# Optimization experiments

Hardware: AMD Instinct MI355X
Metric: run time of the kernel (lower is better)

The kernel has to match this reference:

```python
import jax, jax.numpy as jnp
import numpy as np

N_NODES = 100000
N_EDGES = 1600000
IN, HID, OUT = 32, 32, 16


def setup_inputs() -> dict:
    key = jax.random.key(0)
    ks = jax.random.split(key, 8)
    return {
        "features": jax.random.normal(ks[0], (N_NODES, IN), dtype=jnp.float32),
        "src": jax.random.randint(ks[1], (N_EDGES,), 0, N_NODES, dtype=jnp.int32),
        "dst": jax.random.randint(ks[2], (N_EDGES,), 0, N_NODES, dtype=jnp.int32),
        "edge_weight": jax.random.uniform(ks[3], (N_EDGES,), dtype=jnp.float32),
        "W1": jax.random.normal(ks[4], (IN, HID), dtype=jnp.float32) * 0.1,
        "b1": jnp.zeros((HID,), dtype=jnp.float32),
        "W2": jax.random.normal(ks[5], (HID, OUT), dtype=jnp.float32) * 0.1,
        "b2": jnp.zeros((OUT,), dtype=jnp.float32),
    }


def _graph_conv(h, W, b, src, dst, edge_weight, norm_src, norm_dst, n):
    # DGL GraphConv, norm='both', with edge_weight (u_mul_e aggregation)
    h = h * norm_src[:, None]          # out-degree^-0.5 on source side
    h = h @ W                          # dense transform (tiny GEMM)
    m = h[src] * edge_weight[:, None]  # gather + edge weighting  [E, d]
    agg = jax.ops.segment_sum(m, dst, num_segments=n)  # scatter-add SpMM
    return agg * norm_dst[:, None] + b # in-degree^-0.5 + bias


def reference(features, src, dst, edge_weight, W1, b1, W2, b2):
    n = features.shape[0]
    ones_e = jnp.ones_like(edge_weight)
    deg_out = jnp.clip(jax.ops.segment_sum(ones_e, src, num_segments=n), 1.0)
    deg_in = jnp.clip(jax.ops.segment_sum(ones_e, dst, num_segments=n), 1.0)
    norm_src = deg_out ** -0.5
    norm_dst = deg_in ** -0.5
    h = _graph_conv(features, W1, b1, src, dst, edge_weight, norm_src, norm_dst, n)
    h = jax.nn.relu(h)
    # dropout is identity in eval mode
    h = _graph_conv(h, W2, b2, src, dst, edge_weight, norm_src, norm_dst, n)
    return h
```

## Files before the change

### kernel.cpp

```cpp
#include <hip/hip_runtime.h>
#include <hip/hip_fp16.h>


#define NB   391
#define CAPB 5504
#define EPB  4096

__device__ __forceinline__ long nt_load_i64(const long* p) {
    return __builtin_nontemporal_load(p);
}

__global__ __launch_bounds__(1024) void partition_kernel(
        const int* __restrict__ src, const int* __restrict__ dst,
        const float* __restrict__ ew,
        int* __restrict__ g_cur_d, int* __restrict__ g_cur_s,
        int2* __restrict__ pack_part, unsigned char* __restrict__ src_part, int m) {
    __shared__ int hist_d[NB], hist_s[NB];
    __shared__ int lbase_d[NB], lbase_s[NB];
    __shared__ int gbase_d[NB], gbase_s[NB];
    __shared__ int cur_d[NB], cur_s[NB];
    __shared__ int woffd[16], woffs[16];
    __shared__ long stage[EPB];
    __shared__ unsigned short dbuck[EPB];
    __shared__ unsigned char  sstage[EPB];
    __shared__ unsigned short sbuck[EPB];
    int t = threadIdx.x, lane = t & 63, w = t >> 6;
    for (int i = t; i < NB; i += 1024) {
        hist_d[i] = 0; hist_s[i] = 0; cur_d[i] = 0; cur_s[i] = 0;
    }
    __syncthreads();
    int base_e = blockIdx.x * EPB;
    int total = m - base_e; if (total > EPB) total = EPB;
    int es[4], ed[4]; float wv[4];
#pragma unroll
    for (int k = 0; k < 4; k++) {
        int e = base_e + k * 1024 + t;
        if (e < m) { es[k] = src[e]; ed[k] = dst[e]; wv[k] = ew[e]; }
        else ed[k] = -1;
    }
#pragma unroll
    for (int k = 0; k < 4; k++) {
        if (ed[k] >= 0) {
            atomicAdd(&hist_d[ed[k] >> 8], 1);
            atomicAdd(&hist_s[es[k] >> 8], 1);
        }
    }
    __syncthreads();
    int hvd = (t < NB) ? hist_d[t] : 0;
    int hvs = (t < NB) ? hist_s[t] : 0;
    int vd = hvd, vs = hvs;
#pragma unroll
    for (int off = 1; off < 64; off <<= 1) {
        int ud = __shfl_up(vd, off, 64);
        int us = __shfl_up(vs, off, 64);
        if (lane >= off) { vd += ud; vs += us; }
    }
    if (lane == 63) { woffd[w] = vd; woffs[w] = vs; }
    __syncthreads();
    if (t < 64) {
        int sd = (t < 16) ? woffd[t] : 0;
        int ss = (t < 16) ? woffs[t] : 0;
        int od = sd, os = ss;
#pragma unroll
        for (int off = 1; off < 16; off <<= 1) {
            int ud = __shfl_up(sd, off, 64);
            int us = __shfl_up(ss, off, 64);
            if (lane >= off) { sd += ud; ss += us; }
        }
        if (t < 16) { woffd[t] = sd - od; woffs[t] = ss - os; }
    }
    __syncthreads();
    if (t < NB) {
        lbase_d[t] = vd + woffd[w] - hvd;
        lbase_s[t] = vs + woffs[w] - hvs;
    }
    for (int i = t; i < NB; i += 1024) {
        int c = hist_d[i];
        gbase_d[i] = i * CAPB + (c ? atomicAdd(&g_cur_d[i], c) : 0);
        c = hist_s[i];
        gbase_s[i] = i * CAPB + (c ? atomicAdd(&g_cur_s[i], c) : 0);
    }
    __syncthreads();
#pragma unroll
    for (int k = 0; k < 4; k++) {
        if (ed[k] >= 0) {
            int d = ed[k], s = es[k];
            int bd = d >> 8;
            int r = atomicAdd(&cur_d[bd], 1);
            int pos = lbase_d[bd] + r;
            stage[pos] = (long)(unsigned int)(s | ((d & 255) << 20)) |
                         ((long)__float_as_int(wv[k]) << 32);
            dbuck[pos] = (unsigned short)bd;
            int bs = s >> 8;
            int rs = atomicAdd(&cur_s[bs], 1);
            int ps = lbase_s[bs] + rs;
            sstage[ps] = (unsigned char)(s & 255);
            sbuck[ps] = (unsigned short)bs;
        }
    }
    __syncthreads();
    long* packl = (long*)pack_part;
    for (int i = t; i < total; i += 1024) {
        int b = dbuck[i];
        packl[(size_t)gbase_d[b] + (i - lbase_d[b])] = stage[i];
    }
    for (int i = t; i < total; i += 1024) {
        int b = sbuck[i];
        src_part[(size_t)gbase_s[b] + (i - lbase_s[b])] = sstage[i];
    }
}

__global__ __launch_bounds__(1024) void csr_kernel(
                           const int2* __restrict__ pack_part,
                           const unsigned char* __restrict__ src_part,
                           const int* __restrict__ g_cur_d, const int* __restrict__ g_cur_s,
                           const float* __restrict__ feat, const float* __restrict__ W1,
                           int2* __restrict__ csr, int2* __restrict__ rs_cnt,
                           float* __restrict__ norm_src, float* __restrict__ norm_dst,
                           __half* __restrict__ h1, int n) {
    __shared__ int cnt[256];
    __shared__ int rowx[256];
    __shared__ int cur[256];
    __shared__ int cnt_s[256];
    __shared__ float nsrc[256];
    __shared__ float sW1[1024];
    extern __shared__ int2 stage[];
    int t = threadIdx.x, b = blockIdx.x;
    if (t < 256) { cnt[t] = 0; cur[t] = 0; cnt_s[t] = 0; }
    sW1[t] = W1[t];
    __syncthreads();
    int count = g_cur_d[b]; if (count > CAPB) count = CAPB;
    int count_s = g_cur_s[b]; if (count_s > CAPB) count_s = CAPB;
    const int2* p = pack_part + (size_t)b * CAPB;
    const unsigned char* sp = src_part + (size_t)b * CAPB;
    int2 pk[4];
#pragma unroll
    for (int u = 0; u < 4; u++) {
        int e = t + u * 1024;
        if (e < count) { pk[u] = p[e]; atomicAdd(&cnt[pk[u].x >> 20], 1); }
    }
    for (int e = t + 4096; e < count; e += 1024)
        atomicAdd(&cnt[p[e].x >> 20], 1);
    for (int e = t; e < count_s; e += 1024) atomicAdd(&cnt_s[sp[e]], 1);
    __syncthreads();
    if (t < 256) {
        int node = b * 256 + t;
        if (node < n) {
            int cs = cnt_s[t];
            float ns = rsqrtf((float)(cs > 1 ? cs : 1));
            nsrc[t] = ns;
            norm_src[node] = ns;
        } else nsrc[t] = 0.0f;
    }
    if (t < 64) {
        int c0 = cnt[t * 4], c1 = cnt[t * 4 + 1], c2 = cnt[t * 4 + 2], c3 = cnt[t * 4 + 3];
        int tot = c0 + c1 + c2 + c3;
        int incl = tot;
#pragma unroll
        for (int off = 1; off < 64; off <<= 1) {
            int u = __shfl_up(incl, off, 64);
            if (t >= off) incl += u;
        }
        int excl = incl - tot;
        rowx[t * 4]     = excl;
        rowx[t * 4 + 1] = excl + c0;
        rowx[t * 4 + 2] = excl + c0 + c1;
        rowx[t * 4 + 3] = excl + c0 + c1 + c2;
    }
    __syncthreads();
    if (t < 256) {
        int node = b * 256 + t;
        if (node < n) {
            rs_cnt[node] = make_int2(b * CAPB + rowx[t], cnt[t]);
            norm_dst[node] = rsqrtf((float)(cnt[t] > 1 ? cnt[t] : 1));
        }
    }
    __syncthreads();
#pragma unroll
    for (int u = 0; u < 4; u++) {
        int e = t + u * 1024;
        if (e < count) {
            int2 v = pk[u];
            int dl = v.x >> 20;
            int r = atomicAdd(&cur[dl], 1);
            stage[rowx[dl] + r] = make_int2(v.x & 0x1FFFF, v.y);
        }
    }
    for (int e = t + 4096; e < count; e += 1024) {
        int2 v = p[e];
        int dl = v.x >> 20;
        int r = atomicAdd(&cur[dl], 1);
        stage[rowx[dl] + r] = make_int2(v.x & 0x1FFFF, v.y);
    }
    __syncthreads();
    int2* outp = csr + (size_t)b * CAPB;
    for (int e = t; e < count; e += 1024) outp[e] = stage[e];
    __syncthreads();
    float* sF = (float*)stage;
    int node0 = b * 256;
    int lim = n - node0; if (lim > 256) lim = 256; if (lim < 0) lim = 0;
    for (int o = t; o < lim * 32; o += 1024) {
        int i = o >> 5, k = o & 31;
        sF[o] = feat[(size_t)(node0 + i) * 32 + k] * nsrc[i];
    }
    __syncthreads();
    for (int o = t; o < lim * 32; o += 1024) {
        int i = o >> 5, col = o & 31;
        float acc = 0.0f;
#pragma unroll
        for (int k = 0; k < 32; k++) acc += sF[i * 32 + k] * sW1[k * 32 + col];
        h1[(size_t)(node0 + i) * 32 + col] = __float2half(acc);
    }
}

__global__ void gather1_fused_kernel(const __half* __restrict__ h1, const int2* __restrict__ csr,
                                     const int2* __restrict__ rs_cnt,
                                     const float* __restrict__ norm_src, const float* __restrict__ norm_dst,
                                     const float* __restrict__ W2, const float* __restrict__ b1,
                                     __half* __restrict__ h2, int n) {
    __shared__ float sW2[32 * 16];
    __shared__ float sB1[32];
    __shared__ float sX[4][8][33];
    int t = threadIdx.x;
    for (int i = t; i < 512; i += 256) sW2[i] = W2[i];
    if (t < 32) sB1[t] = b1[t];
    __syncthreads();
    int w = t >> 6, lane = t & 63;
    int q = lane >> 3;
    int dq = lane & 7;
    int node = (blockIdx.x * 4 + w) * 8 + q;
    bool valid = node < n;
    int2 rc = valid ? rs_cnt[node] : make_int2(0, 0);
    long base = rc.x;
    int c = rc.y;
    const float2* tv = (const float2*)h1;
    const long* csrl = (const long*)csr;
    float a00=0,a01=0,a02=0,a03=0, a10=0,a11=0,a12=0,a13=0;
    float a20=0,a21=0,a22=0,a23=0, a30=0,a31=0,a32=0,a33=0;
    int j = 0;
    for (; j + 3 < c; j += 4) {
        long q0 = nt_load_i64(csrl + base + j);
        long q1 = nt_load_i64(csrl + base + j + 1);
        long q2 = nt_load_i64(csrl + base + j + 2);
        long q3 = nt_load_i64(csrl + base + j + 3);
        float2 r0 = tv[(size_t)((int)q0 & 0xFFFFF) * 8 + dq];
        float2 r1 = tv[(size_t)((int)q1 & 0xFFFFF) * 8 + dq];
        float2 r2 = tv[(size_t)((int)q2 & 0xFFFFF) * 8 + dq];
        float2 r3 = tv[(size_t)((int)q3 & 0xFFFFF) * 8 + dq];
        float w0 = __int_as_float((int)(q0 >> 32)), w1 = __int_as_float((int)(q1 >> 32));
        float w2 = __int_as_float((int)(q2 >> 32)), w3 = __int_as_float((int)(q3 >> 32));
        float2 l0 = __half22float2(*(__half2*)&r0.x), h0 = __half22float2(*(__half2*)&r0.y);
        float2 l1 = __half22float2(*(__half2*)&r1.x), h1v = __half22float2(*(__half2*)&r1.y);
        float2 l2 = __half22float2(*(__half2*)&r2.x), h2v = __half22float2(*(__half2*)&r2.y);
        float2 l3 = __half22float2(*(__half2*)&r3.x), h3v = __half22float2(*(__half2*)&r3.y);
        a00 += l0.x * w0; a01 += l0.y * w0; a02 += h0.x * w0; a03 += h0.y * w0;
        a10 += l1.x * w1; a11 += l1.y * w1; a12 += h1v.x * w1; a13 += h1v.y * w1;
        a20 += l2.x * w2; a21 += l2.y * w2; a22 += h2v.x * w2; a23 += h2v.y * w2;
        a30 += l3.x * w3; a31 += l3.y * w3; a32 += h3v.x * w3; a33 += h3v.y * w3;
    }
    for (; j < c; j++) {
        long qq = nt_load_i64(csrl + base + j);
        float2 r = tv[(size_t)((int)qq & 0xFFFFF) * 8 + dq];
        float ww = __int_as_float((int)(qq >> 32));
        float2 l = __half22float2(*(__half2*)&r.x), h = __half22float2(*(__half2*)&r.y);
        a00 += l.x * ww; a01 += l.y * ww; a02 += h.x * ww; a03 += h.y * ww;
    }
    float s0 = (a00 + a10) + (a20 + a30);
    float s1 = (a01 + a11) + (a21 + a31);
    float s2 = (a02 + a12) + (a22 + a32);
    float s3 = (a03 + a13) + (a23 + a33);
    if (valid) {
        float nd = norm_dst[node], ns = norm_src[node];
        int d0 = 4 * dq;
        sX[w][q][d0]     = fmaxf(s0 * nd + sB1[d0],     0.0f) * ns;
        sX[w][q][d0 + 1] = fmaxf(s1 * nd + sB1[d0 + 1], 0.0f) * ns;
        sX[w][q][d0 + 2] = fmaxf(s2 * nd + sB1[d0 + 2], 0.0f) * ns;
        sX[w][q][d0 + 3] = fmaxf(s3 * nd + sB1[d0 + 3], 0.0f) * ns;
    }
    if (valid) {
        float o0 = 0.0f, o1 = 0.0f;
        int c0 = 2 * dq, c1 = 2 * dq + 1;
#pragma unroll
        for (int k = 0; k < 32; k++) {
            float x = sX[w][q][k];
            o0 += x * sW2[k * 16 + c0];
            o1 += x * sW2[k * 16 + c1];
        }
        ((__half2*)h2)[(size_t)node * 8 + dq] = __floats2half2_rn(o0, o1);
    }
}

__global__ void gather2_kernel(const __half* __restrict__ h2, const int2* __restrict__ csr,
                               const int2* __restrict__ rs_cnt,
                               const float* __restrict__ norm_dst, const float* __restrict__ b2,
                               float* __restrict__ out, int n) {
    int t = threadIdx.x;
    int w = t >> 6, lane = t & 63;
    int q = lane >> 2;
    int dq = lane & 3;
    int node = (blockIdx.x * 4 + w) * 16 + q;
    bool valid = node < n;
    int2 rc = valid ? rs_cnt[node] : make_int2(0, 0);
    long base = rc.x;
    int c = rc.y;
    const float2* tv = (const float2*)h2;
    const long* csrl = (const long*)csr;
    float a00=0,a01=0,a02=0,a03=0, a10=0,a11=0,a12=0,a13=0;
    float a20=0,a21=0,a22=0,a23=0, a30=0,a31=0,a32=0,a33=0;
    int j = 0;
    for (; j + 3 < c; j += 4) {
        long q0 = nt_load_i64(csrl + base + j);
        long q1 = nt_load_i64(csrl + base + j + 1);
        long q2 = nt_load_i64(csrl + base + j + 2);
        long q3 = nt_load_i64(csrl + base + j + 3);
        float2 r0 = tv[(size_t)((int)q0 & 0xFFFFF) * 4 + dq];
        float2 r1 = tv[(size_t)((int)q1 & 0xFFFFF) * 4 + dq];
        float2 r2 = tv[(size_t)((int)q2 & 0xFFFFF) * 4 + dq];
        float2 r3 = tv[(size_t)((int)q3 & 0xFFFFF) * 4 + dq];
        float w0 = __int_as_float((int)(q0 >> 32)), w1 = __int_as_float((int)(q1 >> 32));
        float w2 = __int_as_float((int)(q2 >> 32)), w3 = __int_as_float((int)(q3 >> 32));
        float2 l0 = __half22float2(*(__half2*)&r0.x), h0 = __half22float2(*(__half2*)&r0.y);
        float2 l1 = __half22float2(*(__half2*)&r1.x), h1v = __half22float2(*(__half2*)&r1.y);
        float2 l2 = __half22float2(*(__half2*)&r2.x), h2v = __half22float2(*(__half2*)&r2.y);
        float2 l3 = __half22float2(*(__half2*)&r3.x), h3v = __half22float2(*(__half2*)&r3.y);
        a00 += l0.x * w0; a01 += l0.y * w0; a02 += h0.x * w0; a03 += h0.y * w0;
        a10 += l1.x * w1; a11 += l1.y * w1; a12 += h1v.x * w1; a13 += h1v.y * w1;
        a20 += l2.x * w2; a21 += l2.y * w2; a22 += h2v.x * w2; a23 += h2v.y * w2;
        a30 += l3.x * w3; a31 += l3.y * w3; a32 += h3v.x * w3; a33 += h3v.y * w3;
    }
    for (; j < c; j++) {
        long qq = nt_load_i64(csrl + base + j);
        float2 r = tv[(size_t)((int)qq & 0xFFFFF) * 4 + dq];
        float ww = __int_as_float((int)(qq >> 32));
        float2 l = __half22float2(*(__half2*)&r.x), h = __half22float2(*(__half2*)&r.y);
        a00 += l.x * ww; a01 += l.y * ww; a02 += h.x * ww; a03 += h.y * ww;
    }
    if (valid) {
        float nd = norm_dst[node];
        int d0 = 4 * dq;
        float4 o;
        o.x = ((a00 + a10) + (a20 + a30)) * nd + b2[d0];
        o.y = ((a01 + a11) + (a21 + a31)) * nd + b2[d0 + 1];
        o.z = ((a02 + a12) + (a22 + a32)) * nd + b2[d0 + 2];
        o.w = ((a03 + a13) + (a23 + a33)) * nd + b2[d0 + 3];
        ((float4*)out)[(size_t)node * 4 + dq] = o;
    }
}

extern "C" void kernel_launch(void* const* d_in, const int* in_sizes, int n_in,
                              void* d_out, int out_size, void* d_ws, size_t ws_size,
                              hipStream_t stream) {
    const float* feat = (const float*)d_in[0];
    const int*   src  = (const int*)d_in[1];
    const int*   dst  = (const int*)d_in[2];
    const float* ew   = (const float*)d_in[3];
    const float* W1   = (const float*)d_in[4];
    const float* b1   = (const float*)d_in[5];
    const float* W2   = (const float*)d_in[6];
    const float* b2   = (const float*)d_in[7];
    float* out = (float*)d_out;

    const int n = in_sizes[0] / 32;
    const int m = in_sizes[1];

    char* wsb = (char*)d_ws;
    int2*   pack_part = (int2*)wsb;
    int2*   csr       = pack_part + (size_t)NB * CAPB;
    __half* h1        = (__half*)(csr + (size_t)NB * CAPB);
    __half* h2        = h1 + 32 * (size_t)n;
    float*  norm_src  = (float*)(h2 + 16 * (size_t)n);
    float*  norm_dst  = norm_src + n;
    int2*   rs_cnt    = (int2*)(norm_dst + n);
    int*    g_cur_d   = (int*)(rs_cnt + n);
    int*    g_cur_s   = g_cur_d + NB;
    unsigned char* src_part = (unsigned char*)(g_cur_s + NB);

    hipMemsetAsync(g_cur_d, 0, 2 * NB * sizeof(int), stream);

    partition_kernel<<<(m + EPB - 1) / EPB, 1024, 0, stream>>>(src, dst, ew, g_cur_d, g_cur_s,
                                                               pack_part, src_part, m);
    csr_kernel<<<NB, 1024, CAPB * sizeof(int2), stream>>>(pack_part, src_part, g_cur_d, g_cur_s,
                                                          feat, W1, csr, rs_cnt,
                                                          norm_src, norm_dst, h1, n);
    gather1_fused_kernel<<<(n + 31) / 32, 256, 0, stream>>>(h1, csr, rs_cnt,
                                                            norm_src, norm_dst, W2, b1, h2, n);
    gather2_kernel<<<(n + 63) / 64, 256, 0, stream>>>(h2, csr, rs_cnt, norm_dst, b2, out, n);
}
```

Before: 186.8 us.

## Fuse GCN pipeline into one cooperative persistent kernel with LDS-resident CSR

Replaces the four separate kernels (partition, CSR build, two gather layers) with a single cooperative kernel of 256 persistent blocks separated by grid-wide syncs. Each block owns two destination buckets and keeps their CSR chains, degree counts and norms in LDS, so the global CSR, rs_cnt and norm arrays are no longer written or read. Layer 2 also runs the W2 transform inside the block. This removes launch gaps and global round-trips, at the cost of large dynamic LDS (about 88 KB) per block, fewer blocks in flight for the latency-bound gathers, and grid-sync overhead.

```diff
diff --git a/kernel.cpp b/kernel.cpp
--- a/kernel.cpp
+++ b/kernel.cpp
@@ -1,388 +1,401 @@
 #include <hip/hip_runtime.h>
 #include <hip/hip_fp16.h>
+#include <hip/hip_cooperative_groups.h>
+
+namespace cg = cooperative_groups;
 
 
 #define NB   391
 #define CAPB 5504
 #define EPB  4096
-
-__device__ __forceinline__ long nt_load_i64(const long* p) {
-    return __builtin_nontemporal_load(p);
-}
-
-__global__ __launch_bounds__(1024) void partition_kernel(
+#define NBLK 256
+#define TPB  1024
+#define UNIB (2 * CAPB * 8)
+
+__global__ __launch_bounds__(TPB, 4) void gcn_mega(
         const int* __restrict__ src, const int* __restrict__ dst,
-        const float* __restrict__ ew,
+        const float* __restrict__ ew, const float* __restrict__ feat,
+        const float* __restrict__ W1, const float* __restrict__ b1,
+        const float* __restrict__ W2, const float* __restrict__ b2,
         int* __restrict__ g_cur_d, int* __restrict__ g_cur_s,
-        int2* __restrict__ pack_part, unsigned char* __restrict__ src_part, int m) {
+        int2* __restrict__ pack_part, unsigned char* __restrict__ src_part,
+        __half* __restrict__ h1, __half* __restrict__ h2,
+        float* __restrict__ out, int n, int m) {
+    extern __shared__ __align__(16) char uni[];
     __shared__ int hist_d[NB], hist_s[NB];
     __shared__ int lbase_d[NB], lbase_s[NB];
     __shared__ int gbase_d[NB], gbase_s[NB];
     __shared__ int cur_d[NB], cur_s[NB];
     __shared__ int woffd[16], woffs[16];
-    __shared__ long stage[EPB];
-    __shared__ unsigned short dbuck[EPB];
-    __shared__ unsigned char  sstage[EPB];
-    __shared__ unsigned short sbuck[EPB];
-    int t = threadIdx.x, lane = t & 63, w = t >> 6;
-    for (int i = t; i < NB; i += 1024) {
-        hist_d[i] = 0; hist_s[i] = 0; cur_d[i] = 0; cur_s[i] = 0;
-    }
-    __syncthreads();
-    int base_e = blockIdx.x * EPB;
-    int total = m - base_e; if (total > EPB) total = EPB;
-    int es[4], ed[4]; float wv[4];
-#pragma unroll
-    for (int k = 0; k < 4; k++) {
-        int e = base_e + k * 1024 + t;
-        if (e < m) { es[k] = src[e]; ed[k] = dst[e]; wv[k] = ew[e]; }
-        else ed[k] = -1;
-    }
-#pragma unroll
-    for (int k = 0; k < 4; k++) {
-        if (ed[k] >= 0) {
-            atomicAdd(&hist_d[ed[k] >> 8], 1);
-            atomicAdd(&hist_s[es[k] >> 8], 1);
+    __shared__ int cnt[2][256], rowx[2][256], cura[256], cnt_s[256];
+    __shared__ float nsrc[2][256], ndst[2][256];
+    __shared__ float sW1[1024], sW2[512], sB1[32], sB2[16];
+    __shared__ float sX[16][8][33];
+
+    cg::grid_group grid = cg::this_grid();
+    const int t = threadIdx.x, lane = t & 63, w = t >> 6;
+    const int bi = blockIdx.x;
+
+    sW1[t] = W1[t];
+    if (t < 512) sW2[t] = W2[t];
+    if (t < 32)  sB1[t] = b1[t];
+    if (t < 16)  sB2[t] = b2[t];
+
+    {
+        long* stageP = (long*)uni;
+        unsigned short* dbuck = (unsigned short*)(uni + 32768);
+        unsigned char*  sstg  = (unsigned char*)(uni + 40960);
+        unsigned short* sbuck = (unsigned short*)(uni + 45056);
+        for (int chunk = bi; chunk * EPB < m; chunk += NBLK) {
+            for (int i = t; i < NB; i += TPB) {
+                hist_d[i] = 0; hist_s[i] = 0; cur_d[i] = 0; cur_s[i] = 0;
+            }
+            __syncthreads();
+            int base_e = chunk * EPB;
+            int total = m - base_e; if (total > EPB) total = EPB;
+            int es[4], ed[4]; float wv[4];
+#pragma unroll
+            for (int k = 0; k < 4; k++) {
+                int e = base_e + k * TPB + t;
+                if (e < m) { es[k] = src[e]; ed[k] = dst[e]; wv[k] = ew[e]; }
+                else ed[k] = -1;
+            }
+#pragma unroll
+            for (int k = 0; k < 4; k++) {
+                if (ed[k] >= 0) {
+                    atomicAdd(&hist_d[ed[k] >> 8], 1);
+                    atomicAdd(&hist_s[es[k] >> 8], 1);
+                }
+            }
+            __syncthreads();
+            int hvd = (t < NB) ? hist_d[t] : 0;
+            int hvs = (t < NB) ? hist_s[t] : 0;
+            int vd = hvd, vs = hvs;
+#pragma unroll
+            for (int off = 1; off < 64; off <<= 1) {
+                int ud = __shfl_up(vd, off, 64);
+                int us = __shfl_up(vs, off, 64);
+                if (lane >= off) { vd += ud; vs += us; }
+            }
+            if (lane == 63) { woffd[w] = vd; woffs[w] = vs; }
+            __syncthreads();
+            if (t < 64) {
+                int sd = (t < 16) ? woffd[t] : 0;
+                int ss = (t < 16) ? woffs[t] : 0;
+                int od = sd, os = ss;
+#pragma unroll
+                for (int off = 1; off < 16; off <<= 1) {
+                    int ud = __shfl_up(sd, off, 64);
+                    int us = __shfl_up(ss, off, 64);
+                    if (lane >= off) { sd += ud; ss += us; }
+                }
+                if (t < 16) { woffd[t] = sd - od; woffs[t] = ss - os; }
+            }
+            __syncthreads();
+            if (t < NB) {
+                lbase_d[t] = vd + woffd[w] - hvd;
+                lbase_s[t] = vs + woffs[w] - hvs;
+            }
+            for (int i = t; i < NB; i += TPB) {
+                int c = hist_d[i];
+                gbase_d[i] = i * CAPB + (c ? atomicAdd(&g_cur_d[i], c) : 0);
+                c = hist_s[i];
+                gbase_s[i] = i * CAPB + (c ? atomicAdd(&g_cur_s[i], c) : 0);
+            }
+            __syncthreads();
+#pragma unroll
+            for (int k = 0; k < 4; k++) {
+                if (ed[k] >= 0) {
+                    int d = ed[k], s = es[k];
+                    int bd = d >> 8;
+                    int r = atomicAdd(&cur_d[bd], 1);
+                    int pos = lbase_d[bd] + r;
+                    stageP[pos] = (long)(unsigned int)(s | ((d & 255) << 20)) |
+                                  ((long)__float_as_int(wv[k]) << 32);
+                    dbuck[pos] = (unsigned short)bd;
+                    int bs = s >> 8;
+                    int rs = atomicAdd(&cur_s[bs], 1);
+                    int ps = lbase_s[bs] + rs;
+                    sstg[ps] = (unsigned char)(s & 255);
+                    sbuck[ps] = (unsigned short)bs;
+                }
+            }
+            __syncthreads();
+            long* packl = (long*)pack_part;
+            for (int i = t; i < total; i += TPB) {
+                int b = dbuck[i];
+                packl[(size_t)gbase_d[b] + (i - lbase_d[b])] = stageP[i];
+            }
+            for (int i = t; i < total; i += TPB) {
+                int b = sbuck[i];
+                src_part[(size_t)gbase_s[b] + (i - lbase_s[b])] = sstg[i];
+            }
+            __syncthreads();
         }
     }
-    __syncthreads();
-    int hvd = (t < NB) ? hist_d[t] : 0;
-    int hvs = (t < NB) ? hist_s[t] : 0;
-    int vd = hvd, vs = hvs;
-#pragma unroll
-    for (int off = 1; off < 64; off <<= 1) {
-        int ud = __shfl_up(vd, off, 64);
-        int us = __shfl_up(vs, off, 64);
-        if (lane >= off) { vd += ud; vs += us; }
-    }
-    if (lane == 63) { woffd[w] = vd; woffs[w] = vs; }
-    __syncthreads();
-    if (t < 64) {
-        int sd = (t < 16) ? woffd[t] : 0;
-        int ss = (t < 16) ? woffs[t] : 0;
-        int od = sd, os = ss;
-#pragma unroll
-        for (int off = 1; off < 16; off <<= 1) {
-            int ud = __shfl_up(sd, off, 64);
-            int us = __shfl_up(ss, off, 64);
-            if (lane >= off) { sd += ud; ss += us; }
-        }
-        if (t < 16) { woffd[t] = sd - od; woffs[t] = ss - os; }
-    }
-    __syncthreads();
-    if (t < NB) {
-        lbase_d[t] = vd + woffd[w] - hvd;
-        lbase_s[t] = vs + woffs[w] - hvs;
-    }
-    for (int i = t; i < NB; i += 1024) {
-        int c = hist_d[i];
-        gbase_d[i] = i * CAPB + (c ? atomicAdd(&g_cur_d[i], c) : 0);
-        c = hist_s[i];
-        gbase_s[i] = i * CAPB + (c ? atomicAdd(&g_cur_s[i], c) : 0);
-    }
-    __syncthreads();
-#pragma unroll
-    for (int k = 0; k < 4; k++) {
-        if (ed[k] >= 0) {
-            int d = ed[k], s = es[k];
-            int bd = d >> 8;
-            int r = atomicAdd(&cur_d[bd], 1);
-            int pos = lbase_d[bd] + r;
-            stage[pos] = (long)(unsigned int)(s | ((d & 255) << 20)) |
-                         ((long)__float_as_int(wv[k]) << 32);
-            dbuck[pos] = (unsigned short)bd;
-            int bs = s >> 8;
-            int rs = atomicAdd(&cur_s[bs], 1);
-            int ps = lbase_s[bs] + rs;
-            sstage[ps] = (unsigned char)(s & 255);
-            sbuck[ps] = (unsigned short)bs;
+    grid.sync();
+
+    const int b0 = bi * 2;
+    const int nb_own = (b0 >= NB) ? 0 : ((b0 + 1 < NB) ? 2 : 1);
+
+    {
+        float* sF = (float*)uni;
+        for (int lb = 0; lb < nb_own; lb++) {
+            const int b = b0 + lb;
+            if (t < 256) cnt_s[t] = 0;
+            __syncthreads();
+            int count_s = g_cur_s[b]; if (count_s > CAPB) count_s = CAPB;
+            const unsigned char* sp = src_part + (size_t)b * CAPB;
+            for (int e = t; e < count_s; e += TPB) atomicAdd(&cnt_s[sp[e]], 1);
+            __syncthreads();
+            const int node0 = b * 256;
+            if (t < 256) {
+                int cs = cnt_s[t];
+                nsrc[lb][t] = ((node0 + t) < n) ? rsqrtf((float)(cs > 1 ? cs : 1)) : 0.0f;
+            }
+            __syncthreads();
+            int lim = n - node0; if (lim > 256) lim = 256; if (lim < 0) lim = 0;
+            for (int o = t; o < lim * 32; o += TPB) {
+                int i = o >> 5, k = o & 31;
+                sF[o] = feat[(size_t)(node0 + i) * 32 + k] * nsrc[lb][i];
+            }
+            __syncthreads();
+            for (int o = t; o < lim * 32; o += TPB) {
+                int i = o >> 5, col = o & 31;
+                float acc = 0.0f;
+#pragma unroll
+                for (int k = 0; k < 32; k++) acc += sF[i * 32 + k] * sW1[k * 32 + col];
+                h1[(size_t)(node0 + i) * 32 + col] = __float2half(acc);
+            }
+            __syncthreads();
         }
     }
-    __syncthreads();
-    long* packl = (long*)pack_part;
-    for (int i = t; i < total; i += 1024) {
-        int b = dbuck[i];
-        packl[(size_t)gbase_d[b] + (i - lbase_d[b])] = stage[i];
-    }
-    for (int i = t; i < total; i += 1024) {
-        int b = sbuck[i];
-        src_part[(size_t)gbase_s[b] + (i - lbase_s[b])] = sstage[i];
-    }
-}
-
-__global__ __launch_bounds__(1024) void csr_kernel(
-                           const int2* __restrict__ pack_part,
-                           const unsigned char* __restrict__ src_part,
-                           const int* __restrict__ g_cur_d, const int* __restrict__ g_cur_s,
-                           const float* __restrict__ feat, const float* __restrict__ W1,
-                           int2* __restrict__ csr, int2* __restrict__ rs_cnt,
-                           float* __restrict__ norm_src, float* __restrict__ norm_dst,
-                           __half* __restrict__ h1, int n) {
-    __shared__ int cnt[256];
-    __shared__ int rowx[256];
-    __shared__ int cur[256];
-    __shared__ int cnt_s[256];
-    __shared__ float nsrc[256];
-    __shared__ float sW1[1024];
-    extern __shared__ int2 stage[];
-    int t = threadIdx.x, b = blockIdx.x;
-    if (t < 256) { cnt[t] = 0; cur[t] = 0; cnt_s[t] = 0; }
-    sW1[t] = W1[t];
-    __syncthreads();
-    int count = g_cur_d[b]; if (count > CAPB) count = CAPB;
-    int count_s = g_cur_s[b]; if (count_s > CAPB) count_s = CAPB;
-    const int2* p = pack_part + (size_t)b * CAPB;
-    const unsigned char* sp = src_part + (size_t)b * CAPB;
-    int2 pk[4];
-#pragma unroll
-    for (int u = 0; u < 4; u++) {
-        int e = t + u * 1024;
-        if (e < count) { pk[u] = p[e]; atomicAdd(&cnt[pk[u].x >> 20], 1); }
-    }
-    for (int e = t + 4096; e < count; e += 1024)
-        atomicAdd(&cnt[p[e].x >> 20], 1);
-    for (int e = t; e < count_s; e += 1024) atomicAdd(&cnt_s[sp[e]], 1);
-    __syncthreads();
-    if (t < 256) {
-        int node = b * 256 + t;
-        if (node < n) {
-            int cs = cnt_s[t];
-            float ns = rsqrtf((float)(cs > 1 ? cs : 1));
-            nsrc[t] = ns;
-            norm_src[node] = ns;
-        } else nsrc[t] = 0.0f;
-    }
-    if (t < 64) {
-        int c0 = cnt[t * 4], c1 = cnt[t * 4 + 1], c2 = cnt[t * 4 + 2], c3 = cnt[t * 4 + 3];
-        int tot = c0 + c1 + c2 + c3;
-        int incl = tot;
-#pragma unroll
-        for (int off = 1; off < 64; off <<= 1) {
-            int u = __shfl_up(incl, off, 64);
-            if (t >= off) incl += u;
-        }
-        int excl = incl - tot;
-        rowx[t * 4]     = excl;
-        rowx[t * 4 + 1] = excl + c0;
-        rowx[t * 4 + 2] = excl + c0 + c1;
-        rowx[t * 4 + 3] = excl + c0 + c1 + c2;
-    }
-    __syncthreads();
-    if (t < 256) {
-        int node = b * 256 + t;
-        if (node < n) {
-            rs_cnt[node] = make_int2(b * CAPB + rowx[t], cnt[t]);
-            norm_dst[node] = rsqrtf((float)(cnt[t] > 1 ? cnt[t] : 1));
+
+    {
+        int2* chains = (int2*)uni;
+        for (int lb = 0; lb < nb_own; lb++) {
+            const int b = b0 + lb;
+            if (t < 256) { cnt[lb][t] = 0; cura[t] = 0; }
+            __syncthreads();
+            int count = g_cur_d[b]; if (count > CAPB) count = CAPB;
+            const int2* p = pack_part + (size_t)b * CAPB;
+            int2 pk[4];
+#pragma unroll
+            for (int u = 0; u < 4; u++) {
+                int e = t + u * TPB;
+                if (e < count) { pk[u] = p[e]; atomicAdd(&cnt[lb][pk[u].x >> 20], 1); }
+            }
+            for (int e = t + 4 * TPB; e < count; e += TPB)
+                atomicAdd(&cnt[lb][p[e].x >> 20], 1);
+            __syncthreads();
+            if (t < 64) {
+                int c0 = cnt[lb][t * 4], c1 = cnt[lb][t * 4 + 1];
+                int c2 = cnt[lb][t * 4 + 2], c3 = cnt[lb][t * 4 + 3];
+                int tot = c0 + c1 + c2 + c3;
+                int incl = tot;
+#pragma unroll
+                for (int off = 1; off < 64; off <<= 1) {
+                    int u = __shfl_up(incl, off, 64);
+                    if (t >= off) incl += u;
+                }
+                int excl = incl - tot;
+                rowx[lb][t * 4]     = excl;
+                rowx[lb][t * 4 + 1] = excl + c0;
+                rowx[lb][t * 4 + 2] = excl + c0 + c1;
+                rowx[lb][t * 4 + 3] = excl + c0 + c1 + c2;
+            }
+            __syncthreads();
+            if (t < 256) {
+                int c0 = cnt[lb][t];
+                ndst[lb][t] = rsqrtf((float)(c0 > 1 ? c0 : 1));
+            }
+            int2* ch = chains + lb * CAPB;
+#pragma unroll
+            for (int u = 0; u < 4; u++) {
+                int e = t + u * TPB;
+                if (e < count) {
+                    int2 v = pk[u];
+                    int dl = v.x >> 20;
+                    int r = atomicAdd(&cura[dl], 1);
+                    ch[rowx[lb][dl] + r] = make_int2(v.x & 0x1FFFF, v.y);
+                }
+            }
+            for (int e = t + 4 * TPB; e < count; e += TPB) {
+                int2 v = p[e];
+                int dl = v.x >> 20;
+                int r = atomicAdd(&cura[dl], 1);
+                ch[rowx[lb][dl] + r] = make_int2(v.x & 0x1FFFF, v.y);
+            }
+            __syncthreads();
         }
     }
-    __syncthreads();
-#pragma unroll
-    for (int u = 0; u < 4; u++) {
-        int e = t + u * 1024;
-        if (e < count) {
-            int2 v = pk[u];
-            int dl = v.x >> 20;
-            int r = atomicAdd(&cur[dl], 1);
-            stage[rowx[dl] + r] = make_int2(v.x & 0x1FFFF, v.y);
+    grid.sync();
+
+    {
+        const int q = lane >> 3, dq = lane & 7;
+        const float2* tv = (const float2*)h1;
+        const int2* chains = (const int2*)uni;
+        for (int lb = 0; lb < nb_own; lb++) {
+            const int b = b0 + lb;
+            const int node0 = b * 256;
+            const int2* ch = chains + lb * CAPB;
+            for (int pp = 0; pp < 2; pp++) {
+                int nl = pp * 128 + w * 8 + q;
+                int node = node0 + nl;
+                bool valid = node < n;
+                int base = rowx[lb][nl];
+                int c = valid ? cnt[lb][nl] : 0;
+                float a00=0,a01=0,a02=0,a03=0, a10=0,a11=0,a12=0,a13=0;
+                float a20=0,a21=0,a22=0,a23=0, a30=0,a31=0,a32=0,a33=0;
+                int j = 0;
+                for (; j + 3 < c; j += 4) {
+                    long q0 = *(const long*)(ch + base + j);
+                    long q1 = *(const long*)(ch + base + j + 1);
+                    long q2 = *(const long*)(ch + base + j + 2);
+                    long q3 = *(const long*)(ch + base + j + 3);
+                    float2 r0 = tv[(size_t)((int)q0 & 0xFFFFF) * 8 + dq];
+                    float2 r1 = tv[(size_t)((int)q1 & 0xFFFFF) * 8 + dq];
+                    float2 r2 = tv[(size_t)((int)q2 & 0xFFFFF) * 8 + dq];
+                    float2 r3 = tv[(size_t)((int)q3 & 0xFFFFF) * 8 + dq];
+                    float w0 = __int_as_float((int)(q0 >> 32)), w1 = __int_as_float((int)(q1 >> 32));
+                    float w2 = __int_as_float((int)(q2 >> 32)), w3 = __int_as_float((int)(q3 >> 32));
+                    float2 l0 = __half22float2(*(__half2*)&r0.x), h0 = __half22float2(*(__half2*)&r0.y);
+                    float2 l1 = __half22float2(*(__half2*)&r1.x), h1v = __half22float2(*(__half2*)&r1.y);
+                    float2 l2 = __half22float2(*(__half2*)&r2.x), h2v = __half22float2(*(__half2*)&r2.y);
+                    float2 l3 = __half22float2(*(__half2*)&r3.x), h3v = __half22float2(*(__half2*)&r3.y);
+                    a00 += l0.x * w0; a01 += l0.y * w0; a02 += h0.x * w0; a03 += h0.y * w0;
+                    a10 += l1.x * w1; a11 += l1.y * w1; a12 += h1v.x * w1; a13 += h1v.y * w1;
+                    a20 += l2.x * w2; a21 += l2.y * w2; a22 += h2v.x * w2; a23 += h2v.y * w2;
+                    a30 += l3.x * w3; a31 += l3.y * w3; a32 += h3v.x * w3; a33 += h3v.y * w3;
+                }
+                for (; j < c; j++) {
+                    long qq = *(const long*)(ch + base + j);
+                    float2 r = tv[(size_t)((int)qq & 0xFFFFF) * 8 + dq];
+                    float ww = __int_as_float((int)(qq >> 32));
+                    float2 l = __half22float2(*(__half2*)&r.x), h = __half22float2(*(__half2*)&r.y);
+                    a00 += l.x * ww; a01 += l.y * ww; a02 += h.x * ww; a03 += h.y * ww;
+                }
+                float s0 = (a00 + a10) + (a20 + a30);
+                float s1 = (a01 + a11) + (a21 + a31);
+                float s2 = (a02 + a12) + (a22 + a32);
+                float s3 = (a03 + a13) + (a23 + a33);
+                if (valid) {
+                    float nd = ndst[lb][nl], ns = nsrc[lb][nl];
+                    int d0 = 4 * dq;
+                    sX[w][q][d0]     = fmaxf(s0 * nd + sB1[d0],     0.0f) * ns;
+                    sX[w][q][d0 + 1] = fmaxf(s1 * nd + sB1[d0 + 1], 0.0f) * ns;
+                    sX[w][q][d0 + 2] = fmaxf(s2 * nd + sB1[d0 + 2], 0.0f) * ns;
+                    sX[w][q][d0 + 3] = fmaxf(s3 * nd + sB1[d0 + 3], 0.0f) * ns;
+                }
+                if (valid) {
+                    float o0 = 0.0f, o1 = 0.0f;
+                    int c0 = 2 * dq, c1 = 2 * dq + 1;
+#pragma unroll
+                    for (int k = 0; k < 32; k++) {
+                        float x = sX[w][q][k];
+                        o0 += x * sW2[k * 16 + c0];
+                        o1 += x * sW2[k * 16 + c1];
+                    }
+                    ((__half2*)h2)[(size_t)node * 8 + dq] = __floats2half2_rn(o0, o1);
+                }
+            }
         }
     }
-    for (int e = t + 4096; e < count; e += 1024) {
-        int2 v = p[e];
-        int dl = v.x >> 20;
-        int r = atomicAdd(&cur[dl], 1);
-        stage[rowx[dl] + r] = make_int2(v.x & 0x1FFFF, v.y);
-    }
-    __syncthreads();
-    int2* outp = csr + (size_t)b * CAPB;
-    for (int e = t; e < count; e += 1024) outp[e] = stage[e];
-    __syncthreads();
-    float* sF = (float*)stage;
-    int node0 = b * 256;
-    int lim = n - node0; if (lim > 256) lim = 256; if (lim < 0) lim = 0;
-    for (int o = t; o < lim * 32; o += 1024) {
-        int i = o >> 5, k = o & 31;
-        sF[o] = feat[(size_t)(node0 + i) * 32 + k] * nsrc[i];
-    }
-    __syncthreads();
-    for (int o = t; o < lim * 32; o += 1024) {
-        int i = o >> 5, col = o & 31;
-        float acc = 0.0f;
-#pragma unroll
-        for (int k = 0; k < 32; k++) acc += sF[i * 32 + k] * sW1[k * 32 + col];
-        h1[(size_t)(node0 + i) * 32 + col] = __float2half(acc);
-    }
-}
-
-__global__ void gather1_fused_kernel(const __half* __restrict__ h1, const int2* __restrict__ csr,
-                                     const int2* __restrict__ rs_cnt,
-                                     const float* __restrict__ norm_src, const float* __restrict__ norm_dst,
-                                     const float* __restrict__ W2, const float* __restrict__ b1,
-                                     __half* __restrict__ h2, int n) {
-    __shared__ float sW2[32 * 16];
-    __shared__ float sB1[32];
-    __shared__ float sX[4][8][33];
-    int t = threadIdx.x;
-    for (int i = t; i < 512; i += 256) sW2[i] = W2[i];
-    if (t < 32) sB1[t] = b1[t];
-    __syncthreads();
-    int w = t >> 6, lane = t & 63;
-    int q = lane >> 3;
-    int dq = lane & 7;
-    int node = (blockIdx.x * 4 + w) * 8 + q;
-    bool valid = node < n;
-    int2 rc = valid ? rs_cnt[node] : make_int2(0, 0);
-    long base = rc.x;
-    int c = rc.y;
-    const float2* tv = (const float2*)h1;
-    const long* csrl = (const long*)csr;
-    float a00=0,a01=0,a02=0,a03=0, a10=0,a11=0,a12=0,a13=0;
-    float a20=0,a21=0,a22=0,a23=0, a30=0,a31=0,a32=0,a33=0;
-    int j = 0;
-    for (; j + 3 < c; j += 4) {
-        long q0 = nt_load_i64(csrl + base + j);
-        long q1 = nt_load_i64(csrl + base + j + 1);
-        long q2 = nt_load_i64(csrl + base + j + 2);
-        long q3 = nt_load_i64(csrl + base + j + 3);
-        float2 r0 = tv[(size_t)((int)q0 & 0xFFFFF) * 8 + dq];
-        float2 r1 = tv[(size_t)((int)q1 & 0xFFFFF) * 8 + dq];
-        float2 r2 = tv[(size_t)((int)q2 & 0xFFFFF) * 8 + dq];
-        float2 r3 = tv[(size_t)((int)q3 & 0xFFFFF) * 8 + dq];
-        float w0 = __int_as_float((int)(q0 >> 32)), w1 = __int_as_float((int)(q1 >> 32));
-        float w2 = __int_as_float((int)(q2 >> 32)), w3 = __int_as_float((int)(q3 >> 32));
-        float2 l0 = __half22float2(*(__half2*)&r0.x), h0 = __half22float2(*(__half2*)&r0.y);
-        float2 l1 = __half22float2(*(__half2*)&r1.x), h1v = __half22float2(*(__half2*)&r1.y);
-        float2 l2 = __half22float2(*(__half2*)&r2.x), h2v = __half22float2(*(__half2*)&r2.y);
-        float2 l3 = __half22float2(*(__half2*)&r3.x), h3v = __half22float2(*(__half2*)&r3.y);
-        a00 += l0.x * w0; a01 += l0.y * w0; a02 += h0.x * w0; a03 += h0.y * w0;
-        a10 += l1.x * w1; a11 += l1.y * w1; a12 += h1v.x * w1; a13 += h1v.y * w1;
-        a20 += l2.x * w2; a21 += l2.y * w2; a22 += h2v.x * w2; a23 += h2v.y * w2;
-        a30 += l3.x * w3; a31 += l3.y * w3; a32 += h3v.x * w3; a33 += h3v.y * w3;
-    }
-    for (; j < c; j++) {
-        long qq = nt_load_i64(csrl + base + j);
-        float2 r = tv[(size_t)((int)qq & 0xFFFFF) * 8 + dq];
-        float ww = __int_as_float((int)(qq >> 32));
-        float2 l = __half22float2(*(__half2*)&r.x), h = __half22float2(*(__half2*)&r.y);
-        a00 += l.x * ww; a01 += l.y * ww; a02 += h.x * ww; a03 += h.y * ww;
-    }
-    float s0 = (a00 + a10) + (a20 + a30);
-    float s1 = (a01 + a11) + (a21 + a31);
-    float s2 = (a02 + a12) + (a22 + a32);
-    float s3 = (a03 + a13) + (a23 + a33);
-    if (valid) {
-        float nd = norm_dst[node], ns = norm_src[node];
-        int d0 = 4 * dq;
-        sX[w][q][d0]     = fmaxf(s0 * nd + sB1[d0],     0.0f) * ns;
-        sX[w][q][d0 + 1] = fmaxf(s1 * nd + sB1[d0 + 1], 0.0f) * ns;
-        sX[w][q][d0 + 2] = fmaxf(s2 * nd + sB1[d0 + 2], 0.0f) * ns;
-        sX[w][q][d0 + 3] = fmaxf(s3 * nd + sB1[d0 + 3], 0.0f) * ns;
-    }
-    if (valid) {
-        float o0 = 0.0f, o1 = 0.0f;
-        int c0 = 2 * dq, c1 = 2 * dq + 1;
-#pragma unroll
-        for (int k = 0; k < 32; k++) {
-            float x = sX[w][q][k];
-            o0 += x * sW2[k * 16 + c0];
-            o1 += x * sW2[k * 16 + c1];
+    grid.sync();
+
+    {
+        const int q = lane >> 2, dq = lane & 3;
+        const float2* tv = (const float2*)h2;
+        const int2* chains = (const int2*)uni;
+        for (int lb = 0; lb < nb_own; lb++) {
+            const int b = b0 + lb;
+            const int node0 = b * 256;
+            const int2* ch = chains + lb * CAPB;
+            int nl = w * 16 + q;
+            int node = node0 + nl;
+            bool valid = node < n;
+            int base = rowx[lb][nl];
+            int c = valid ? cnt[lb][nl] : 0;
+            float a00=0,a01=0,a02=0,a03=0, a10=0,a11=0,a12=0,a13=0;
+            float a20=0,a21=0,a22=0,a23=0, a30=0,a31=0,a32=0,a33=0;
+            int j = 0;
+            for (; j + 3 < c; j += 4) {
+                long q0 = *(const long*)(ch + base + j);
+                long q1 = *(const long*)(ch + base + j + 1);
+                long q2 = *(const long*)(ch + base + j + 2);
+                long q3 = *(const long*)(ch + base + j + 3);
+                float2 r0 = tv[(size_t)((int)q0 & 0xFFFFF) * 4 + dq];
+                float2 r1 = tv[(size_t)((int)q1 & 0xFFFFF) * 4 + dq];
+                float2 r2 = tv[(size_t)((int)q2 & 0xFFFFF) * 4 + dq];
+                float2 r3 = tv[(size_t)((int)q3 & 0xFFFFF) * 4 + dq];
+                float w0 = __int_as_float((int)(q0 >> 32)), w1 = __int_as_float((int)(q1 >> 32));
+                float w2 = __int_as_float((int)(q2 >> 32)), w3 = __int_as_float((int)(q3 >> 32));
+                float2 l0 = __half22float2(*(__half2*)&r0.x), h0 = __half22float2(*(__half2*)&r0.y);
+                float2 l1 = __half22float2(*(__half2*)&r1.x), h1v = __half22float2(*(__half2*)&r1.y);
+                float2 l2 = __half22float2(*(__half2*)&r2.x), h2v = __half22float2(*(__half2*)&r2.y);
+                float2 l3 = __half22float2(*(__half2*)&r3.x), h3v = __half22float2(*(__half2*)&r3.y);
+                a00 += l0.x * w0; a01 += l0.y * w0; a02 += h0.x * w0; a03 += h0.y * w0;
+                a10 += l1.x * w1; a11 += l1.y * w1; a12 += h1v.x * w1; a13 += h1v.y * w1;
+                a20 += l2.x * w2; a21 += l2.y * w2; a22 += h2v.x * w2; a23 += h2v.y * w2;
+                a30 += l3.x * w3; a31 += l3.y * w3; a32 += h3v.x * w3; a33 += h3v.y * w3;
+            }
+            for (; j < c; j++) {
+                long qq = *(const long*)(ch + base + j);
+                float2 r = tv[(size_t)((int)qq & 0xFFFFF) * 4 + dq];
+                float ww = __int_as_float((int)(qq >> 32));
+                float2 l = __half22float2(*(__half2*)&r.x), h = __half22float2(*(__half2*)&r.y);
+                a00 += l.x * ww; a01 += l.y * ww; a02 += h.x * ww; a03 += h.y * ww;
+            }
+            if (valid) {
+                float nd = ndst[lb][nl];
+                int d0 = 4 * dq;
+                float4 o;
+                o.x = ((a00 + a10) + (a20 + a30)) * nd + sB2[d0];
+                o.y = ((a01 + a11) + (a21 + a31)) * nd + sB2[d0 + 1];
+                o.z = ((a02 + a12) + (a22 + a32)) * nd + sB2[d0 + 2];
+                o.w = ((a03 + a13) + (a23 + a33)) * nd + sB2[d0 + 3];
+                ((float4*)out)[(size_t)node * 4 + dq] = o;
+            }
         }
-        ((__half2*)h2)[(size_t)node * 8 + dq] = __floats2half2_rn(o0, o1);
-    }
-}
-
-__global__ void gather2_kernel(const __half* __restrict__ h2, const int2* __restrict__ csr,
-                               const int2* __restrict__ rs_cnt,
-                               const float* __restrict__ norm_dst, const float* __restrict__ b2,
-                               float* __restrict__ out, int n) {
-    int t = threadIdx.x;
-    int w = t >> 6, lane = t & 63;
-    int q = lane >> 2;
-    int dq = lane & 3;
-    int node = (blockIdx.x * 4 + w) * 16 + q;
-    bool valid = node < n;
-    int2 rc = valid ? rs_cnt[node] : make_int2(0, 0);
-    long base = rc.x;
-    int c = rc.y;
-    const float2* tv = (const float2*)h2;
-    const long* csrl = (const long*)csr;
-    float a00=0,a01=0,a02=0,a03=0, a10=0,a11=0,a12=0,a13=0;
-    float a20=0,a21=0,a22=0,a23=0, a30=0,a31=0,a32=0,a33=0;
-    int j = 0;
-    for (; j + 3 < c; j += 4) {
-        long q0 = nt_load_i64(csrl + base + j);
-        long q1 = nt_load_i64(csrl + base + j + 1);
-        long q2 = nt_load_i64(csrl + base + j + 2);
-        long q3 = nt_load_i64(csrl + base + j + 3);
-        float2 r0 = tv[(size_t)((int)q0 & 0xFFFFF) * 4 + dq];
-        float2 r1 = tv[(size_t)((int)q1 & 0xFFFFF) * 4 + dq];
-        float2 r2 = tv[(size_t)((int)q2 & 0xFFFFF) * 4 + dq];
-        float2 r3 = tv[(size_t)((int)q3 & 0xFFFFF) * 4 + dq];
-        float w0 = __int_as_float((int)(q0 >> 32)), w1 = __int_as_float((int)(q1 >> 32));
-        float w2 = __int_as_float((int)(q2 >> 32)), w3 = __int_as_float((int)(q3 >> 32));
-        float2 l0 = __half22float2(*(__half2*)&r0.x), h0 = __half22float2(*(__half2*)&r0.y);
-        float2 l1 = __half22float2(*(__half2*)&r1.x), h1v = __half22float2(*(__half2*)&r1.y);
-        float2 l2 = __half22float2(*(__half2*)&r2.x), h2v = __half22float2(*(__half2*)&r2.y);
-        float2 l3 = __half22float2(*(__half2*)&r3.x), h3v = __half22float2(*(__half2*)&r3.y);
-        a00 += l0.x * w0; a01 += l0.y * w0; a02 += h0.x * w0; a03 += h0.y * w0;
-        a10 += l1.x * w1; a11 += l1.y * w1; a12 += h1v.x * w1; a13 += h1v.y * w1;
-        a20 += l2.x * w2; a21 += l2.y * w2; a22 += h2v.x * w2; a23 += h2v.y * w2;
-        a30 += l3.x * w3; a31 += l3.y * w3; a32 += h3v.x * w3; a33 += h3v.y * w3;
-    }
-    for (; j < c; j++) {
-        long qq = nt_load_i64(csrl + base + j);
-        float2 r = tv[(size_t)((int)qq & 0xFFFFF) * 4 + dq];
-        float ww = __int_as_float((int)(qq >> 32));
-        float2 l = __half22float2(*(__half2*)&r.x), h = __half22float2(*(__half2*)&r.y);
-        a00 += l.x * ww; a01 += l.y * ww; a02 += h.x * ww; a03 += h.y * ww;
-    }
-    if (valid) {
-        float nd = norm_dst[node];
-        int d0 = 4 * dq;
-        float4 o;
-        o.x = ((a00 + a10) + (a20 + a30)) * nd + b2[d0];
-        o.y = ((a01 + a11) + (a21 + a31)) * nd + b2[d0 + 1];
-        o.z = ((a02 + a12) + (a22 + a32)) * nd + b2[d0 + 2];
-        o.w = ((a03 + a13) + (a23 + a33)) * nd + b2[d0 + 3];
-        ((float4*)out)[(size_t)node * 4 + dq] = o;
     }
 }
 
 extern "C" void kernel_launch(void* const* d_in, const int* in_sizes, int n_in,
                               void* d_out, int out_size, void* d_ws, size_t ws_size,
                               hipStream_t stream) {
-    const float* feat = (const float*)d_in[0];
-    const int*   src  = (const int*)d_in[1];
-    const int*   dst  = (const int*)d_in[2];
-    const float* ew   = (const float*)d_in[3];
-    const float* W1   = (const float*)d_in[4];
-    const float* b1   = (const float*)d_in[5];
-    const float* W2   = (const float*)d_in[6];
-    const float* b2   = (const float*)d_in[7];
+    const int* src_p   = (const int*)d_in[1];
+    const int* dst_p   = (const int*)d_in[2];
+    const float* ew_p  = (const float*)d_in[3];
+    const float* feat  = (const float*)d_in[0];
+    const float* W1    = (const float*)d_in[4];
+    const float* b1    = (const float*)d_in[5];
+    const float* W2    = (const float*)d_in[6];
+    const float* b2    = (const float*)d_in[7];
     float* out = (float*)d_out;
 
-    const int n = in_sizes[0] / 32;
-    const int m = in_sizes[1];
+    int n = in_sizes[0] / 32;
+    int m = in_sizes[1];
 
     char* wsb = (char*)d_ws;
     int2*   pack_part = (int2*)wsb;
-    int2*   csr       = pack_part + (size_t)NB * CAPB;
-    __half* h1        = (__half*)(csr + (size_t)NB * CAPB);
+    __half* h1        = (__half*)(pack_part + (size_t)NB * CAPB);
     __half* h2        = h1 + 32 * (size_t)n;
-    float*  norm_src  = (float*)(h2 + 16 * (size_t)n);
-    float*  norm_dst  = norm_src + n;
-    int2*   rs_cnt    = (int2*)(norm_dst + n);
-    int*    g_cur_d   = (int*)(rs_cnt + n);
+    int*    g_cur_d   = (int*)(h2 + 16 * (size_t)n);
     int*    g_cur_s   = g_cur_d + NB;
     unsigned char* src_part = (unsigned char*)(g_cur_s + NB);
 
     hipMemsetAsync(g_cur_d, 0, 2 * NB * sizeof(int), stream);
 
-    partition_kernel<<<(m + EPB - 1) / EPB, 1024, 0, stream>>>(src, dst, ew, g_cur_d, g_cur_s,
-                                                               pack_part, src_part, m);
-    csr_kernel<<<NB, 1024, CAPB * sizeof(int2), stream>>>(pack_part, src_part, g_cur_d, g_cur_s,
-                                                          feat, W1, csr, rs_cnt,
-                                                          norm_src, norm_dst, h1, n);
-    gather1_fused_kernel<<<(n + 31) / 32, 256, 0, stream>>>(h1, csr, rs_cnt,
-                                                            norm_src, norm_dst, W2, b1, h2, n);
-    gather2_kernel<<<(n + 63) / 64, 256, 0, stream>>>(h2, csr, rs_cnt, norm_dst, b2, out, n);
+    hipFuncSetAttribute((const void*)gcn_mega,
+                        hipFuncAttributeMaxDynamicSharedMemorySize, UNIB);
+
+    void* args[] = {
+        (void*)&src_p, (void*)&dst_p, (void*)&ew_p, (void*)&feat,
+        (void*)&W1, (void*)&b1, (void*)&W2, (void*)&b2,
+        (void*)&g_cur_d, (void*)&g_cur_s,
+        (void*)&pack_part, (void*)&src_part,
+        (void*)&h1, (void*)&h2, (void*)&out, (void*)&n, (void*)&m
+    };
+    hipLaunchCooperativeKernel((const void*)gcn_mega, dim3(NBLK), dim3(TPB),
+                               args, (unsigned int)UNIB, stream);
 }
```

After: 276.2 us. 47.8% more time.
